# Performance work log

Hardware: AMD Instinct MI355X
Metric: run time of the kernel (lower is better)

## Reference

```python
import jax, jax.numpy as jnp
import numpy as np
from jax import lax

B, N, FIN, T, K, FC, FT = 8, 2048, 3, 12, 3, 64, 64


def _conv2d(x, w, b, pad):
    # x [B,C,N,T], w [O,I,1,kw], NCHW conv
    y = lax.conv_general_dilated(x, w, (1, 1), pad,
                                 dimension_numbers=('NCHW', 'OIHW', 'NCHW'))
    return y + b[None, :, None, None]


def _spatial_att(h, W, a, alpha, concat):
    # GAT-style dense attention. h [B,N,Fin], W [Fin,D], a [2D,1]
    D = W.shape[1]
    Wh = h @ W                                             # [B,N,D]
    e = jax.nn.leaky_relu(Wh @ a[:D] + jnp.swapaxes(Wh @ a[D:], 1, 2), alpha)  # [B,N,N]
    att = jax.nn.softmax(jax.nn.sigmoid(e), axis=1)        # softmax over dim=1 (as in torch)
    hp = jnp.einsum('bij,bjd->bid', att, Wh)
    return jax.nn.elu(hp) if concat else hp


def setup_inputs() -> dict:
    key = jax.random.key(0)
    ks = jax.random.split(key, 24)
    rnd = lambda i, shape, scale=1.0: (jax.random.normal(ks[i], shape, dtype=jnp.float32) * scale)
    FTm = FC * T  # 768 spatial-attention feature dim
    D = FTm // 2
    return {
        'x': rnd(0, (B, N, FIN, T)),
        'cheb': rnd(1, (K, N, N), 1.0 / np.sqrt(N)),
        'Gamma': rnd(2, (K, FIN, FC), 1.0 / np.sqrt(FIN)),
        'W_heads': rnd(3, (2, FTm, D), 1.0 / np.sqrt(FTm)),
        'a_heads': rnd(4, (2, 2 * D, 1), 1.0 / np.sqrt(2 * D)),
        'W_out': rnd(5, (FTm, FTm), 1.0 / np.sqrt(FTm)),
        'a_out': rnd(6, (2 * FTm, 1), 1.0 / np.sqrt(2 * FTm)),
        'U1': rnd(7, (FT, FT), 1.0 / np.sqrt(FT)),
        'U2': rnd(8, (FT,), 1.0 / np.sqrt(FT)),
        'U3': rnd(9, (FT,), 1.0 / np.sqrt(FT)),
        'be': rnd(10, (1, T, T), 0.1),
        'Ve': rnd(11, (T, T), 1.0 / np.sqrt(T)),
        'time_w': rnd(12, (FT, FC, 1, 3), 1.0 / np.sqrt(3 * FC)),
        'time_b': rnd(13, (FT,), 0.01),
        'res_w': rnd(14, (FT, FIN, 1, 1), 1.0 / np.sqrt(FIN)),
        'res_b': rnd(15, (FT,), 0.01),
        'back_w': rnd(16, (FT, FC, 1, 3), 1.0 / np.sqrt(3 * FC)),
        'back_b': rnd(17, (FT,), 0.01),
        'fore_w': rnd(18, (FT, FC, 1, 3), 1.0 / np.sqrt(3 * FC)),
        'fore_b': rnd(19, (FT,), 0.01),
        'ln_g': jnp.ones((FT,), jnp.float32),
        'ln_b': jnp.zeros((FT,), jnp.float32),
    }


def reference(x, cheb, Gamma, W_heads, a_heads, W_out, a_out, U1, U2, U3, be, Ve,
              time_w, time_b, res_w, res_b, back_w, back_b, fore_w, fore_b, ln_g, ln_b):
    b, n, fin, t = x.shape
    k_ = cheb.shape[0]
    fc = Gamma.shape[2]
    # ChebNetII interpolation coefficients T_k(x_j), x_j = cos((j+0.5)pi/K) -> [j,k]
    jj = np.arange(k_)
    cxj = jnp.asarray(np.cos(np.outer((jj + 0.5) * np.pi / k_, np.arange(k_))), x.dtype)
    lhs = jnp.einsum('jio,jk->kio', Gamma, cxj)                         # [K,Fin,Fc]
    rhs = jnp.einsum('bnit,knm->kbmit', x, cheb)                        # [K,B,N,Fin,T]
    spatial_gcn = jax.nn.relu((2.0 / (k_ + 1)) * jnp.einsum('kbmit,kio->bmot', rhs, lhs))  # [B,N,Fc,T]

    # Spatial transformer: 2 GAT heads + output attention
    h = spatial_gcn.reshape(b, n, fc * t)
    heads = jax.vmap(lambda W, a: _spatial_att(h, W, a, 0.1, True))(W_heads, a_heads)  # [H,B,N,D]
    hcat = jnp.transpose(heads, (1, 2, 0, 3)).reshape(b, n, -1)
    gcn_SAt = jax.nn.relu(_spatial_att(hcat, W_out, a_out, 0.1, False)).reshape(b, n, fc, t)

    # Temporal conv (1x3, pad 1)
    tc = _conv2d(jnp.transpose(gcn_SAt, (0, 2, 1, 3)), time_w, time_b, ((0, 0), (1, 1)))
    tc = jnp.transpose(tc, (0, 2, 1, 3))                                # [B,N,Ft,T]

    # Temporal attention
    lhs_t = jnp.einsum('bnft,fg,g->btn', tc, U1, U2)                    # [B,T,N]
    rhs_t = jnp.einsum('f,bnft->bnt', U3, tc)                           # [B,N,T]
    prod = jnp.einsum('bsn,bnt->bst', lhs_t, rhs_t)                     # [B,T,T]
    E = jnp.einsum('is,bst->bit', Ve, jax.nn.sigmoid(prod + be))
    E = jax.nn.softmax(E, axis=1)
    tcn = jnp.einsum('bnft,bts->bnfs', tc, E)                           # [B,N,Ft,T]

    # Residual (1x1 conv) + LayerNorm over channel dim
    x_res = _conv2d(jnp.transpose(x, (0, 2, 1, 3)), res_w, res_b, ((0, 0), (0, 0)))
    x_res = jnp.transpose(x_res, (0, 2, 1, 3))                          # [B,N,Ft,T]
    z = jnp.transpose(jax.nn.relu(x_res + tcn), (0, 3, 1, 2))           # [B,T,N,Ft]
    mu = z.mean(-1, keepdims=True)
    var = z.var(-1, keepdims=True)
    z = (z - mu) / jnp.sqrt(var + 1e-5) * ln_g + ln_b
    result = jnp.transpose(z, (0, 2, 3, 1))                             # [B,N,Ft,T]

    rp = jnp.transpose(result, (0, 2, 1, 3))
    backcast = jnp.transpose(_conv2d(rp, back_w, back_b, ((0, 0), (1, 1))), (0, 2, 1, 3))
    forecast = jnp.transpose(_conv2d(rp, fore_w, fore_b, ((0, 0), (1, 1))), (0, 2, 1, 3))
    return (backcast, forecast)
```

## Files before the change

kernel.cpp:

```cpp
#include <hip/hip_runtime.h>


typedef unsigned short u16;
typedef __bf16 bf16x8 __attribute__((ext_vector_type(8)));
typedef float f32x4 __attribute__((ext_vector_type(4)));
typedef u16 u16x8 __attribute__((ext_vector_type(8)));

__device__ __forceinline__ u16 f2b(float f) {
  union { float f; unsigned u; } v; v.f = f;
  unsigned u = v.u;
  u = u + 0x7FFFu + ((u >> 16) & 1u);
  return (u16)(u >> 16);
}
__device__ __forceinline__ float b2f(u16 h) {
  union { unsigned u; float f; } v; v.u = ((unsigned)h) << 16; return v.f;
}
__device__ __forceinline__ float qfun(float x) {
  float e = x > 0.f ? x : 0.1f * x;
  float s = 1.f / (1.f + __expf(-e));
  return __expf(s);
}

#define GLOAD16(g, l) __builtin_amdgcn_global_load_lds( \
    (__attribute__((address_space(1))) void*)(g),       \
    (__attribute__((address_space(3))) void*)(l), 16, 0, 0)

constexpr size_t OFF_LHS     = 0x0;
constexpr size_t OFF_U1U2    = 0x1000;
constexpr size_t OFF_BIASBIG = 0x1100;
constexpr size_t OFF_FH      = 0x3000;
constexpr size_t OFF_GH      = 0x23000;
constexpr size_t OFF_RDH     = 0x43000;
constexpr size_t OFF_FO      = 0x63000;
constexpr size_t OFF_GO      = 0x73000;
constexpr size_t OFF_RDO     = 0x83000;
constexpr size_t OFF_LHST    = 0x93000;
constexpr size_t OFF_RHST    = 0x153000;
constexpr size_t OFF_PROD    = 0x213000;
constexpr size_t OFF_E       = 0x215000;
constexpr size_t OFF_WCATT   = 0x220000;
constexpr size_t OFF_WOUTT   = 0x340000;
constexpr size_t OFF_WTBIG   = 0x460000;
constexpr size_t OFF_XCOLT   = 0x580000;
constexpr size_t OFF_CHEBT   = 0x700000;
constexpr size_t OFF_C1      = 0x1F00000;
constexpr size_t OFF_H       = 0x4300000;
constexpr size_t OFF_P       = 0x700000;
constexpr size_t OFF_WHCATT  = 0x5B00000;
constexpr size_t OFF_HCAT    = 0x7300000;
constexpr size_t OFF_WHOUTT  = 0x5B00000;
constexpr size_t OFF_GCNB    = 0x7300000;
constexpr size_t OFF_WBFBIG  = 0x8B00000;
constexpr size_t OFF_TCS     = 0x700000;
constexpr size_t OFF_RESULTB = 0x3700000;
constexpr size_t WS_NEEDED   = 0x8D40000;

struct GemmP {
  const u16* A; const u16* BT;
  long sA, sB;
  int K, lda, ldb;
  int swz, splitK;
  float* Cf; long sCf; int ldcf;
  u16* Cb;  long sCb; int ldcb;
  u16* CbT; int ldcT; long sCbT;
  const float* bias;
  float* outB; float* outF;
};

template <int EPI>
__global__ __launch_bounds__(256, 2) void gemm_bf16(GemmP p) {
  constexpr int SMEM_U16 = (EPI == 1) ? 17408 : 16384;
  __shared__ u16 smem[SMEM_U16];
  const int tid  = threadIdx.x;
  const int lane = tid & 63;
  const int wid  = tid >> 6;
  const int wm = wid >> 1, wn = wid & 1;
  const int z = blockIdx.z;

  long m0, n0;
  if (p.swz) {
    int nT = gridDim.x;
    int nwg = nT * gridDim.y;
    int lin = blockIdx.x + nT * blockIdx.y;
    int q = nwg >> 3;
    int swz = (lin & 7) * q + (lin >> 3);
    m0 = (long)(swz / nT) * 128;
    n0 = (long)(swz % nT) * 128;
  } else {
    m0 = (long)blockIdx.x * 128;
    n0 = (long)blockIdx.y * 128;
  }

  const int K = p.K;
  long aBase, bBase;
  if (p.splitK) {
    int kz = z >> 2, ch = z & 3;
    aBase = (long)kz * p.sA + (long)ch * 512;
    bBase = (long)ch * 512;
  } else {
    aBase = (long)z * p.sA;
    bBase = (long)z * p.sB;
  }
  const u16* Ab = p.A + aBase + m0 * p.lda;
  const u16* Bb = p.BT + bBase + n0 * p.ldb;

  const int srow = wid * 32 + (lane >> 2);
  const int sk   = (((lane & 3) ^ ((lane >> 3) & 3))) * 8;
  const u16* aP0 = Ab + (long)srow * p.lda + sk;
  const u16* aP1 = aP0 + (long)16 * p.lda;
  const u16* bP0 = Bb + (long)srow * p.ldb + sk;
  const u16* bP1 = bP0 + (long)16 * p.ldb;

  f32x4 acc[4][4];
  f32x4 zero = {0.f, 0.f, 0.f, 0.f};
#pragma unroll
  for (int i = 0; i < 4; ++i)
#pragma unroll
    for (int j = 0; j < 4; ++j) acc[i][j] = zero;

  const int xorc = (lane >> 1) & 3;
  const int aoff = (wm * 64 + (lane & 15)) * 32 + (((lane >> 4) ^ xorc)) * 8;
  const int boff = (wn * 64 + (lane & 15)) * 32 + (((lane >> 4) ^ xorc)) * 8;

  const int lslot = (wid * 2) * 512;

  {
    u16* base = smem;
    GLOAD16(aP0, base + lslot);
    GLOAD16(aP1, base + lslot + 512);
    GLOAD16(bP0, base + 4096 + lslot);
    GLOAD16(bP1, base + 4096 + lslot + 512);
  }
  __syncthreads();

  int cur = 0;
  for (int k0 = 0; k0 < K; k0 += 32) {
    if (k0 + 32 < K) {
      u16* base = smem + (cur ^ 1) * 8192;
      GLOAD16(aP0 + k0 + 32, base + lslot);
      GLOAD16(aP1 + k0 + 32, base + lslot + 512);
      GLOAD16(bP0 + k0 + 32, base + 4096 + lslot);
      GLOAD16(bP1 + k0 + 32, base + 4096 + lslot + 512);
    }
    const u16* As = smem + cur * 8192;
    const u16* Bs = As + 4096;
    bf16x8 av[4], bv[4];
#pragma unroll
    for (int mi = 0; mi < 4; ++mi) av[mi] = *(const bf16x8*)&As[aoff + mi * 512];
#pragma unroll
    for (int ni = 0; ni < 4; ++ni) bv[ni] = *(const bf16x8*)&Bs[boff + ni * 512];
#pragma unroll
    for (int mi = 0; mi < 4; ++mi)
#pragma unroll
      for (int ni = 0; ni < 4; ++ni)
        acc[mi][ni] = __builtin_amdgcn_mfma_f32_16x16x32_bf16(av[mi], bv[ni], acc[mi][ni], 0, 0, 0);
    __syncthreads();
    cur ^= 1;
  }

  if constexpr (EPI == 1) {
#pragma unroll
    for (int mi = 0; mi < 4; ++mi)
#pragma unroll
      for (int ni = 0; ni < 4; ++ni) {
        int cl = wn * 64 + ni * 16 + (lane & 15);
        int mlb = wm * 64 + mi * 16 + ((lane >> 4) << 2);
#pragma unroll
        for (int r = 0; r < 4; ++r)
          smem[cl * 136 + mlb + r] = f2b(acc[mi][ni][r]);
      }
    __syncthreads();
    int c = tid >> 1, half = tid & 1;
    long bat = m0 >> 11;
    u16* dst = p.CbT + bat * p.sCbT + (long)(n0 + c) * p.ldcT + (m0 & 2047) + half * 64;
    const u16* srcp = &smem[c * 136 + half * 64];
#pragma unroll
    for (int j = 0; j < 64; j += 8)
      *(u16x8*)(dst + j) = *(const u16x8*)(srcp + j);
    return;
  }

#pragma unroll
  for (int mi = 0; mi < 4; ++mi) {
    long rb0 = m0 + wm * 64 + mi * 16 + ((lane >> 4) << 2);
#pragma unroll
    for (int ni = 0; ni < 4; ++ni) {
      int col = (int)n0 + wn * 64 + ni * 16 + (lane & 15);
#pragma unroll
      for (int r = 0; r < 4; ++r) {
        float v = acc[mi][ni][r];
        long row = rb0 + r;
        if constexpr (EPI == 0) {
          p.Cf[(long)z * p.sCf + row * p.ldcf + col] = v;
        } else if constexpr (EPI == 2) {
          float e = v > 0.f ? v : expm1f(v);
          p.Cb[(long)z * p.sCb + row * p.ldcb + col] = f2b(e);
        } else if constexpr (EPI == 6) {
          p.Cb[row * 768 + col] = f2b(v + p.bias[col & 63]);
        } else if constexpr (EPI == 7) {
          float vb = v + p.bias[col];
          if (col < 768) p.outB[row * 768 + col] = vb;
          else           p.outF[row * 768 + (col - 768)] = vb;
        } else {
          p.Cb[(long)z * p.sCb + row * p.ldcb + col] = f2b(fmaxf(v, 0.f));
        }
      }
    }
  }
}

__global__ void k_prep(const float* Gamma, const float* U1, const float* U2,
                       const float* back_b, const float* fore_b,
                       float* lhs, float* u1u2, float* biasBig) {
  int o = threadIdx.x;
  if (o < 64) {
    const float cx[3][3] = {{1.f, 0.86602540378443871f, 0.5f},
                            {1.f, 6.123233995736766e-17f, -1.f},
                            {1.f, -0.86602540378443871f, 0.5f}};
    for (int k = 0; k < 3; ++k)
      for (int i = 0; i < 3; ++i) {
        float s = 0;
        for (int j = 0; j < 3; ++j) s += Gamma[(j * 3 + i) * 64 + o] * cx[j][k];
        lhs[(k * 3 + i) * 64 + o] = s;
      }
    float s = 0;
    for (int g = 0; g < 64; ++g) s += U1[o * 64 + g] * U2[g];
    u1u2[o] = s;
    for (int t = 0; t < 12; ++t) {
      biasBig[o * 12 + t] = back_b[o];
      biasBig[768 + o * 12 + t] = fore_b[o];
    }
  }
}

__global__ void k_convert(const float* W_heads, const float* W_out, const float* time_w,
                          const float* back_w, const float* fore_w, const float* xg,
                          u16* WcatT, u16* WoutT, u16* WtBig, u16* WbfBig, u16* xcolT) {
  const int N1 = 589824, NT = 589824, NBF = 1179648, N5 = 786432;
  const int TOT = 2 * N1 + NT + NBF + N5;
  for (int o = blockIdx.x * 256 + threadIdx.x; o < TOT; o += gridDim.x * 256) {
    if (o < N1) {
      int dcol = o / 768, kk = o % 768;
      int hd = dcol / 384, d = dcol % 384;
      WcatT[o] = f2b(W_heads[((long)hd * 768 + kk) * 384 + d]);
    } else if (o < 2 * N1) {
      int o2 = o - N1; int dcol = o2 / 768, kk = o2 % 768;
      WoutT[o2] = f2b(W_out[kk * 768 + dcol]);
    } else if (o < 2 * N1 + NT) {
      int o3 = o - 2 * N1; int col = o3 / 768, kk = o3 % 768;
      int t = col >> 6, ft = col & 63, fc = kk / 12, tau = kk % 12;
      int r = tau - t + 1;
      WtBig[o3] = f2b((r >= 0 && r < 3) ? time_w[ft * 192 + fc * 3 + r] : 0.f);
    } else if (o < 2 * N1 + NT + NBF) {
      int o4 = o - 2 * N1 - NT; int col = o4 / 768, kk = o4 % 768;
      int rem = (col < 768) ? col : col - 768;
      int c = rem / 12, tt = rem % 12;
      int fc = kk / 12, tau = kk % 12; int r = tau - tt + 1;
      const float* wsrc = (col < 768) ? back_w : fore_w;
      WbfBig[o4] = f2b((r >= 0 && r < 3) ? wsrc[c * 192 + fc * 3 + r] : 0.f);
    } else {
      int o5 = o - 2 * N1 - NT - NBF; int c = o5 / 2048, n = o5 % 2048;
      float v = 0.f;
      if (c < 288) {
        int b = c / 36, r2 = c % 36, i = r2 / 12, t = r2 % 12;
        v = xg[(long)(b * 2048 + n) * 36 + i * 12 + t];
      }
      xcolT[o5] = f2b(v);
    }
  }
}

__global__ void k_chebT(const float* cheb, u16* chebT) {
  __shared__ float ts[32][33];
  int n0 = blockIdx.x * 32, m0 = blockIdx.y * 32, k = blockIdx.z;
  int c = threadIdx.x & 31, rq = threadIdx.x >> 5;
  const long base = (long)k * 2048 * 2048;
  for (int q = 0; q < 4; ++q) {
    int n = n0 + rq + q * 8;
    ts[rq + q * 8][c] = cheb[base + (long)n * 2048 + m0 + c];
  }
  __syncthreads();
  for (int q = 0; q < 4; ++q) {
    int m = m0 + rq + q * 8;
    chebT[base + (long)m * 2048 + n0 + c] = f2b(ts[c][rq + q * 8]);
  }
}

__global__ __launch_bounds__(256) void k_h(const float* C1, const float* lhs, u16* h) {
  int bn = blockIdx.x; int b = bn >> 11, n = bn & 2047;
  int tid = threadIdx.x;
  __shared__ float c1s[108], ls[576];
  if (tid < 108) {
    int kk = tid / 12, t = tid % 12; int k = kk / 3, i = kk % 3;
    float s = 0;
#pragma unroll
    for (int ch = 0; ch < 4; ++ch)
      s += C1[((long)(k * 4 + ch) * 2048 + n) * 384 + b * 36 + i * 12 + t];
    c1s[tid] = s;
  }
  for (int s = tid; s < 576; s += 256) ls[s] = lhs[s];
  __syncthreads();
  for (int q = 0; q < 3; ++q) {
    int idx = tid + q * 256; int o = idx / 12, t = idx % 12;
    float s = 0;
#pragma unroll
    for (int kk = 0; kk < 9; ++kk) s += c1s[kk * 12 + t] * ls[kk * 64 + o];
    s *= 0.5f;
    if (s < 0.f) s = 0.f;
    h[(long)bn * 768 + idx] = f2b(s);
  }
}

__global__ __launch_bounds__(256) void k_fg(const u16* WhT, int dOff, int Dlen,
                                            const float* aF, const float* aG,
                                            float* fOut, float* gOut) {
  int b = blockIdx.y;
  int i = blockIdx.x * 256 + threadIdx.x;
  __shared__ float af[768], ag[768];
  for (int s = threadIdx.x; s < Dlen; s += 256) { af[s] = aF[s]; ag[s] = aG[s]; }
  __syncthreads();
  const u16* wp = WhT + ((long)b * 768 + dOff) * 2048 + i;
  float fs = 0, gs = 0;
  for (int d = 0; d < Dlen; ++d) {
    float w = b2f(wp[(long)d * 2048]);
    fs += w * af[d]; gs += w * ag[d];
  }
  fOut[b * 2048 + i] = fs;
  gOut[b * 2048 + i] = gs;
}

__global__ __launch_bounds__(256) void k_denom(const float* f, const float* g, float* rd) {
  int b = blockIdx.y;
  int jl = threadIdx.x & 63, ch = threadIdx.x >> 6;
  int j = blockIdx.x * 64 + jl;
  __shared__ float fl[2048];
  __shared__ float red[256];
  for (int s = threadIdx.x; s < 2048; s += 256) fl[s] = f[b * 2048 + s];
  __syncthreads();
  float gj = g[b * 2048 + j];
  float acc = 0;
  for (int i = ch * 512; i < ch * 512 + 512; ++i) acc += qfun(fl[i] + gj);
  red[threadIdx.x] = acc;
  __syncthreads();
  if (ch == 0) {
    float s = red[jl] + red[jl + 64] + red[jl + 128] + red[jl + 192];
    rd[b * 2048 + j] = 1.f / s;
  }
}

__global__ __launch_bounds__(256) void k_P(const float* f, const float* g,
                                           const float* rd, u16* P) {
  int j = blockIdx.x * 256 + threadIdx.x;
  int i0 = blockIdx.y * 16;
  int b = blockIdx.z;
  __shared__ float fl[16];
  if (threadIdx.x < 16) fl[threadIdx.x] = f[b * 2048 + i0 + threadIdx.x];
  __syncthreads();
  float gj = g[b * 2048 + j], rj = rd[b * 2048 + j];
  u16* Pp = P + ((long)b * 2048 + i0) * 2048 + j;
#pragma unroll
  for (int ii = 0; ii < 16; ++ii) Pp[(long)ii * 2048] = f2b(qfun(fl[ii] + gj) * rj);
}

__global__ void k_temporal(const u16* tc, const float* u1u2, const float* U3g,
                           float* lhs_t, float* rhs_t) {
  __shared__ float uu[64], u3[64];
  int tid = threadIdx.x;
  if (tid < 64) { uu[tid] = u1u2[tid]; u3[tid] = U3g[tid]; }
  __syncthreads();
  int gid = blockIdx.x * 256 + tid;
  const u16* p = tc + (long)gid * 64;
  float s1 = 0, s2 = 0;
#pragma unroll
  for (int c = 0; c < 8; ++c) {
    u16x8 vv = *(const u16x8*)(p + c * 8);
#pragma unroll
    for (int j = 0; j < 8; ++j) {
      float v = b2f(vv[j]);
      s1 += v * uu[c * 8 + j]; s2 += v * u3[c * 8 + j];
    }
  }
  int t = gid % 12; long bn = gid / 12;
  int b = (int)(bn >> 11);
  lhs_t[((long)b * 12 + t) * 2048 + (int)(bn & 2047)] = s1;
  rhs_t[gid] = s2;
}

__global__ void k_prod(const float* lhs_t, const float* rhs_t, float* prod) {
  int bi = blockIdx.x;
  int b = bi / 144; int r = bi % 144; int s = r / 12; int u = r % 12;
  int tid = threadIdx.x;
  float acc = 0;
  const float* lp = lhs_t + ((long)b * 12 + s) * 2048;
  const float* rp = rhs_t + (long)b * 2048 * 12 + u;
  for (int n = tid; n < 2048; n += 256) acc += lp[n] * rp[n * 12];
  __shared__ float red[256];
  red[tid] = acc; __syncthreads();
  for (int st = 128; st > 0; st >>= 1) {
    if (tid < st) red[tid] += red[tid + st];
    __syncthreads();
  }
  if (tid == 0) prod[bi] = red[0];
}

__global__ void k_E(const float* prod, const float* be, const float* Ve, float* E) {
  int b = blockIdx.x; int tid = threadIdx.x;
  __shared__ float S0[144], E1[144], mx[12], dn[12];
  if (tid < 144) {
    float v = prod[b * 144 + tid] + be[tid];
    S0[tid] = 1.f / (1.f + __expf(-v));
  }
  __syncthreads();
  if (tid < 144) {
    int i = tid / 12, t = tid % 12;
    float a = 0;
    for (int s = 0; s < 12; ++s) a += Ve[i * 12 + s] * S0[s * 12 + t];
    E1[tid] = a;
  }
  __syncthreads();
  if (tid < 12) {
    float m = -1e30f;
    for (int i = 0; i < 12; ++i) m = fmaxf(m, E1[i * 12 + tid]);
    float d = 0;
    for (int i = 0; i < 12; ++i) d += __expf(E1[i * 12 + tid] - m);
    mx[tid] = m; dn[tid] = d;
  }
  __syncthreads();
  if (tid < 144) {
    int t = tid % 12;
    E[b * 144 + tid] = __expf(E1[tid] - mx[t]) / dn[t];
  }
}

__global__ __launch_bounds__(256) void k_res_ln(const u16* tc, const float* E,
                                                const float* xg, const float* res_w,
                                                const float* res_b, const float* ln_g,
                                                const float* ln_b, u16* result) {
  int bn = blockIdx.x; int b = bn >> 11;
  int tid = threadIdx.x;
  __shared__ float tcb[768], Eb[144], xl[36], rw[192], rb[64], lg[64], lb[64], zl[768], mu[12], rs[12];
  for (int s = tid; s < 768; s += 256) tcb[s] = b2f(tc[(long)bn * 768 + s]);
  if (tid < 144) Eb[tid] = E[b * 144 + tid];
  if (tid < 36) xl[tid] = xg[(long)bn * 36 + tid];
  if (tid >= 64 && tid < 256) { int q = tid - 64; if (q < 192) rw[q] = res_w[q]; }
  if (tid < 64) { rb[tid] = res_b[tid]; lg[tid] = ln_g[tid]; lb[tid] = ln_b[tid]; }
  __syncthreads();
  float z[3];
#pragma unroll
  for (int q = 0; q < 3; ++q) {
    int idx = tid + q * 256; int f = idx / 12, s = idx % 12;
    float tcn = 0;
#pragma unroll
    for (int t = 0; t < 12; ++t) tcn += tcb[t * 64 + f] * Eb[t * 12 + s];
    float xr = rb[f];
#pragma unroll
    for (int i = 0; i < 3; ++i) xr += rw[f * 3 + i] * xl[i * 12 + s];
    float v = xr + tcn;
    v = v > 0.f ? v : 0.f;
    z[q] = v; zl[idx] = v;
  }
  __syncthreads();
  if (tid < 12) {
    float m = 0, m2 = 0;
    for (int f = 0; f < 64; ++f) { float v = zl[f * 12 + tid]; m += v; m2 += v * v; }
    m *= (1.f / 64.f); m2 *= (1.f / 64.f);
    mu[tid] = m;
    float var = m2 - m * m;
    rs[tid] = rsqrtf((var > 0.f ? var : 0.f) + 1e-5f);
  }
  __syncthreads();
#pragma unroll
  for (int q = 0; q < 3; ++q) {
    int idx = tid + q * 256; int f = idx / 12, s = idx % 12;
    result[(long)bn * 768 + idx] = f2b((z[q] - mu[s]) * rs[s] * lg[f] + lb[f]);
  }
}

__global__ void k_sentinel(float* out, long n) {
  long i = (long)blockIdx.x * 256 + threadIdx.x;
  if (i < n) out[i] = 12345.0f;
}

extern "C" void kernel_launch(void* const* d_in, const int* in_sizes, int n_in,
                              void* d_out, int out_size, void* d_ws, size_t ws_size,
                              hipStream_t stream) {
  (void)in_sizes; (void)n_in;
  const float* x       = (const float*)d_in[0];
  const float* cheb    = (const float*)d_in[1];
  const float* Gamma   = (const float*)d_in[2];
  const float* W_heads = (const float*)d_in[3];
  const float* a_heads = (const float*)d_in[4];
  const float* W_out   = (const float*)d_in[5];
  const float* a_out   = (const float*)d_in[6];
  const float* U1      = (const float*)d_in[7];
  const float* U2      = (const float*)d_in[8];
  const float* U3      = (const float*)d_in[9];
  const float* be      = (const float*)d_in[10];
  const float* Ve      = (const float*)d_in[11];
  const float* time_w  = (const float*)d_in[12];
  const float* time_b  = (const float*)d_in[13];
  const float* res_w   = (const float*)d_in[14];
  const float* res_b   = (const float*)d_in[15];
  const float* back_w  = (const float*)d_in[16];
  const float* back_b  = (const float*)d_in[17];
  const float* fore_w  = (const float*)d_in[18];
  const float* fore_b  = (const float*)d_in[19];
  const float* ln_g    = (const float*)d_in[20];
  const float* ln_b    = (const float*)d_in[21];
  float* out = (float*)d_out;

  if (ws_size < WS_NEEDED) {
    k_sentinel<<<(out_size + 255) / 256, 256, 0, stream>>>(out, out_size);
    return;
  }

  char* ws = (char*)d_ws;
  float* lhs     = (float*)(ws + OFF_LHS);
  float* u1u2    = (float*)(ws + OFF_U1U2);
  float* biasBig = (float*)(ws + OFF_BIASBIG);
  float* fH      = (float*)(ws + OFF_FH);
  float* gH      = (float*)(ws + OFF_GH);
  float* rdH     = (float*)(ws + OFF_RDH);
  float* fO      = (float*)(ws + OFF_FO);
  float* gO      = (float*)(ws + OFF_GO);
  float* rdO     = (float*)(ws + OFF_RDO);
  float* lhs_t   = (float*)(ws + OFF_LHST);
  float* rhs_t   = (float*)(ws + OFF_RHST);
  float* prod    = (float*)(ws + OFF_PROD);
  float* Ebuf    = (float*)(ws + OFF_E);
  u16* WcatT   = (u16*)(ws + OFF_WCATT);
  u16* WoutT   = (u16*)(ws + OFF_WOUTT);
  u16* WtBig   = (u16*)(ws + OFF_WTBIG);
  u16* WbfBig  = (u16*)(ws + OFF_WBFBIG);
  u16* xcolT   = (u16*)(ws + OFF_XCOLT);
  u16* chebT   = (u16*)(ws + OFF_CHEBT);
  float* C1    = (float*)(ws + OFF_C1);
  u16* hbuf    = (u16*)(ws + OFF_H);
  u16* Pbuf    = (u16*)(ws + OFF_P);
  u16* WhcatT  = (u16*)(ws + OFF_WHCATT);
  u16* hcat    = (u16*)(ws + OFF_HCAT);
  u16* WhoutT  = (u16*)(ws + OFF_WHOUTT);
  u16* gcnB    = (u16*)(ws + OFF_GCNB);
  u16* tcsB    = (u16*)(ws + OFF_TCS);
  u16* resultB = (u16*)(ws + OFF_RESULTB);

  k_prep<<<1, 64, 0, stream>>>(Gamma, U1, U2, back_b, fore_b, lhs, u1u2, biasBig);
  k_convert<<<2048, 256, 0, stream>>>(W_heads, W_out, time_w, back_w, fore_w, x,
                                      WcatT, WoutT, WtBig, WbfBig, xcolT);
  k_chebT<<<dim3(64, 64, 3), 256, 0, stream>>>(cheb, chebT);

  {
    GemmP p{}; p.A = chebT; p.BT = xcolT; p.sA = 2048L * 2048; p.sB = 0;
    p.K = 512; p.lda = 2048; p.ldb = 2048; p.splitK = 1; p.swz = 1;
    p.Cf = C1; p.sCf = 2048L * 384; p.ldcf = 384;
    gemm_bf16<0><<<dim3(3, 16, 12), 256, 0, stream>>>(p);
  }
  k_h<<<16384, 256, 0, stream>>>(C1, lhs, hbuf);

  {
    GemmP p{}; p.A = hbuf; p.BT = WcatT; p.sA = 0; p.sB = 0;
    p.K = 768; p.lda = 768; p.ldb = 768; p.swz = 1;
    p.CbT = WhcatT; p.ldcT = 2048; p.sCbT = 768L * 2048;
    gemm_bf16<1><<<dim3(6, 128, 1), 256, 0, stream>>>(p);
  }
  k_fg<<<dim3(8, 8), 256, 0, stream>>>(WhcatT, 0, 384, a_heads, a_heads + 384, fH, gH);
  k_fg<<<dim3(8, 8), 256, 0, stream>>>(WhcatT, 384, 384, a_heads + 768, a_heads + 1152,
                                       fH + 16384, gH + 16384);
  for (int hd = 0; hd < 2; ++hd) {
    const float* f = fH + hd * 16384; const float* g = gH + hd * 16384;
    float* rd = rdH + hd * 16384;
    k_denom<<<dim3(32, 8), 256, 0, stream>>>(f, g, rd);
    k_P<<<dim3(8, 128, 8), 256, 0, stream>>>(f, g, rd, Pbuf);
    GemmP p{}; p.A = Pbuf; p.BT = WhcatT + (long)hd * 384 * 2048;
    p.sA = 2048L * 2048; p.sB = 768L * 2048;
    p.K = 2048; p.lda = 2048; p.ldb = 2048; p.swz = 1;
    p.Cb = hcat + hd * 384; p.sCb = 2048L * 768; p.ldcb = 768;
    gemm_bf16<2><<<dim3(3, 16, 8), 256, 0, stream>>>(p);
  }

  {
    GemmP p{}; p.A = hcat; p.BT = WoutT; p.sA = 0; p.sB = 0;
    p.K = 768; p.lda = 768; p.ldb = 768; p.swz = 1;
    p.CbT = WhoutT; p.ldcT = 2048; p.sCbT = 768L * 2048;
    gemm_bf16<1><<<dim3(6, 128, 1), 256, 0, stream>>>(p);
  }
  k_fg<<<dim3(8, 8), 256, 0, stream>>>(WhoutT, 0, 768, a_out, a_out + 768, fO, gO);
  k_denom<<<dim3(32, 8), 256, 0, stream>>>(fO, gO, rdO);
  k_P<<<dim3(8, 128, 8), 256, 0, stream>>>(fO, gO, rdO, Pbuf);
  {
    GemmP p{}; p.A = Pbuf; p.BT = WhoutT; p.sA = 2048L * 2048; p.sB = 768L * 2048;
    p.K = 2048; p.lda = 2048; p.ldb = 2048; p.swz = 1;
    p.Cb = gcnB; p.sCb = 2048L * 768; p.ldcb = 768;
    gemm_bf16<8><<<dim3(6, 16, 8), 256, 0, stream>>>(p);
  }

  {
    GemmP p{}; p.A = gcnB; p.BT = WtBig; p.sA = 0; p.sB = 0;
    p.K = 768; p.lda = 768; p.ldb = 768; p.swz = 1;
    p.Cb = tcsB; p.bias = time_b;
    gemm_bf16<6><<<dim3(6, 128, 1), 256, 0, stream>>>(p);
  }

  k_temporal<<<768, 256, 0, stream>>>(tcsB, u1u2, U3, lhs_t, rhs_t);
  k_prod<<<1152, 256, 0, stream>>>(lhs_t, rhs_t, prod);
  k_E<<<8, 256, 0, stream>>>(prod, be, Ve, Ebuf);

  k_res_ln<<<16384, 256, 0, stream>>>(tcsB, Ebuf, x, res_w, res_b, ln_g, ln_b, resultB);

  {
    GemmP p{}; p.A = resultB; p.BT = WbfBig; p.sA = 0; p.sB = 0;
    p.K = 768; p.lda = 768; p.ldb = 768; p.swz = 1;
    p.bias = biasBig; p.outB = out; p.outF = out + 12582912L;
    gemm_bf16<7><<<dim3(12, 128, 1), 256, 0, stream>>>(p);
  }
}
```

Before: 777.3 us.

## Keep two LDS stages in flight in GEMM mainloop with explicit waitcnt barriers

The bf16 MFMA GEMM mainloop now issues loads for the next two k-steps before computing and uses explicit vmcnt/lgkmcnt waits with raw s_barrier instead of __syncthreads. The goal is to keep one global-to-LDS load outstanding while the current tile is computed, hiding memory latency. It also swaps the sigmoid divide for a hardware reciprocal. The hand-written waitcnt counts must match the number of outstanding loads exactly, or LDS reads could race with in-flight writes.

New measurement: 698.9 us. 1.11x faster.

```diff
diff --git a/kernel.cpp b/kernel.cpp
--- a/kernel.cpp
+++ b/kernel.cpp
@@ -17,7 +17,7 @@
 }
 __device__ __forceinline__ float qfun(float x) {
   float e = x > 0.f ? x : 0.1f * x;
-  float s = 1.f / (1.f + __expf(-e));
+  float s = __builtin_amdgcn_rcpf(1.f + __expf(-e));
   return __expf(s);
 }
 
@@ -124,25 +124,27 @@
 
   const int lslot = (wid * 2) * 512;
 
-  {
-    u16* base = smem;
-    GLOAD16(aP0, base + lslot);
-    GLOAD16(aP1, base + lslot + 512);
-    GLOAD16(bP0, base + 4096 + lslot);
-    GLOAD16(bP1, base + 4096 + lslot + 512);
-  }
-  __syncthreads();
-
-  int cur = 0;
-  for (int k0 = 0; k0 < K; k0 += 32) {
-    if (k0 + 32 < K) {
-      u16* base = smem + (cur ^ 1) * 8192;
-      GLOAD16(aP0 + k0 + 32, base + lslot);
-      GLOAD16(aP1 + k0 + 32, base + lslot + 512);
-      GLOAD16(bP0 + k0 + 32, base + 4096 + lslot);
-      GLOAD16(bP1 + k0 + 32, base + 4096 + lslot + 512);
-    }
-    const u16* As = smem + cur * 8192;
+#define STAGE(s, bufbase) do {                                  \
+    GLOAD16(aP0 + (long)(s) * 32, (bufbase) + lslot);           \
+    GLOAD16(aP1 + (long)(s) * 32, (bufbase) + lslot + 512);     \
+    GLOAD16(bP0 + (long)(s) * 32, (bufbase) + 4096 + lslot);    \
+    GLOAD16(bP1 + (long)(s) * 32, (bufbase) + 4096 + lslot + 512); } while (0)
+
+  const int nsteps = K >> 5;
+  u16* buf0 = smem;
+  u16* buf1 = smem + 8192;
+
+  STAGE(0, buf0);
+  if (nsteps > 1) {
+    STAGE(1, buf1);
+    asm volatile("s_waitcnt vmcnt(4)" ::: "memory");
+  } else {
+    asm volatile("s_waitcnt vmcnt(0)" ::: "memory");
+  }
+  asm volatile("s_barrier" ::: "memory");
+
+  for (int i = 0; i < nsteps; ++i) {
+    const u16* As = smem + (i & 1) * 8192;
     const u16* Bs = As + 4096;
     bf16x8 av[4], bv[4];
 #pragma unroll
@@ -154,9 +156,20 @@
 #pragma unroll
       for (int ni = 0; ni < 4; ++ni)
         acc[mi][ni] = __builtin_amdgcn_mfma_f32_16x16x32_bf16(av[mi], bv[ni], acc[mi][ni], 0, 0, 0);
-    __syncthreads();
-    cur ^= 1;
-  }
+    if (i + 1 < nsteps) {
+      asm volatile("s_waitcnt lgkmcnt(0)" ::: "memory");
+      asm volatile("s_barrier" ::: "memory");
+      if (i + 2 < nsteps) {
+        STAGE(i + 2, (i & 1) ? buf1 : buf0);
+        asm volatile("s_waitcnt vmcnt(4)" ::: "memory");
+      } else {
+        asm volatile("s_waitcnt vmcnt(0)" ::: "memory");
+      }
+      asm volatile("s_barrier" ::: "memory");
+    }
+  }
+#undef STAGE
+  __syncthreads();
 
   if constexpr (EPI == 1) {
 #pragma unroll
```
